# Kernel optimization log

Measured on AMD Instinct MI355X. Metric: run time of the kernel, lower is better.

Reference implementation:

```python
import jax, jax.numpy as jnp
import numpy as np

T_START = 0.0
T_END = 1.0
STEPS = 10
HID = 1024
BATCH = 8192


def setup_inputs() -> dict:
    key = jax.random.key(0)
    ks = jax.random.split(key, 7)
    s1 = 1.0 / np.sqrt(HID + 1)
    s2 = 1.0 / np.sqrt(HID)
    return {
        "h": jax.random.normal(ks[0], (BATCH, HID), dtype=jnp.float32),
        "W1": jax.random.uniform(ks[1], (HID + 1, HID), jnp.float32, -s1, s1),
        "b1": jax.random.uniform(ks[2], (HID,), jnp.float32, -s1, s1),
        "W2": jax.random.uniform(ks[3], (HID, HID), jnp.float32, -s2, s2),
        "b2": jax.random.uniform(ks[4], (HID,), jnp.float32, -s2, s2),
        "W3": jax.random.uniform(ks[5], (HID, HID), jnp.float32, -s2, s2),
        "b3": jax.random.uniform(ks[6], (HID,), jnp.float32, -s2, s2),
    }


def reference(h, W1, b1, W2, b2, W3, b3):
    dt = (T_END - T_START) / STEPS

    def dynamics(t, h):
        # concat(h, t*ones) @ W1 == h @ W1[:-1] + t * W1[-1]; keep explicit concat for clarity
        t_vec = jnp.full((h.shape[0], 1), t, dtype=h.dtype)
        x = jnp.concatenate([h, t_vec], axis=1)
        x = jnp.tanh(x @ W1 + b1)
        x = jnp.tanh(x @ W2 + b2)
        return x @ W3 + b3

    def rk4_step(h, t):
        k1 = dynamics(t, h)
        k2 = dynamics(t + dt / 2, h + dt / 2 * k1)
        k3 = dynamics(t + dt / 2, h + dt / 2 * k2)
        k4 = dynamics(t + dt, h + dt * k3)
        return h + dt / 6 * (k1 + 2 * k2 + 2 * k3 + k4), None

    ts = T_START + dt * jnp.arange(STEPS, dtype=h.dtype)
    h_final, _ = jax.lax.scan(rk4_step, h, ts)
    return h_final
```

## Files before the change

### kernel.cpp

```cpp
#include <hip/hip_runtime.h>


typedef __attribute__((ext_vector_type(8))) __bf16 bf16x8;
typedef __attribute__((ext_vector_type(4))) float f32x4;
typedef __attribute__((ext_vector_type(8))) float f32x8;
typedef __attribute__((ext_vector_type(16))) float f32x16;
typedef __attribute__((ext_vector_type(8))) unsigned short us8;
typedef __attribute__((ext_vector_type(4))) int i32x4;
typedef __attribute__((ext_vector_type(8))) int i32x8;
typedef unsigned short ushort_t;
typedef unsigned char u8;

#define SCALE_ONE  0x7F7F7F7Fu
#define SCALE_INV32 0x7A7A7A7Au

#define GLOAD16(gp, lp) \
  __builtin_amdgcn_global_load_lds((const __attribute__((address_space(1))) unsigned int*)(gp), \
                                   (__attribute__((address_space(3))) unsigned int*)(lp), 16, 0, 0)

__device__ __forceinline__ ushort_t f2bf(float f) {
  union { float f; unsigned u; } v; v.f = f;
  unsigned r = v.u + 0x7fffu + ((v.u >> 16) & 1u);
  return (ushort_t)(r >> 16);
}
__device__ __forceinline__ float b2f(ushort_t u) {
  union { unsigned u; float f; } v; v.u = ((unsigned)u) << 16; return v.f;
}
__device__ __forceinline__ float fast_tanh(float x) {
  float e = __expf(2.0f * x);
  return 1.0f - 2.0f * __builtin_amdgcn_rcpf(e + 1.0f);
}
__device__ __forceinline__ uint2 pack_fp8x8(const float* v) {
  int a = __builtin_amdgcn_cvt_pk_fp8_f32(v[0], v[1], 0, false);
  a = __builtin_amdgcn_cvt_pk_fp8_f32(v[2], v[3], a, true);
  int b = __builtin_amdgcn_cvt_pk_fp8_f32(v[4], v[5], 0, false);
  b = __builtin_amdgcn_cvt_pk_fp8_f32(v[6], v[7], b, true);
  return make_uint2((unsigned)a, (unsigned)b);
}
__device__ __forceinline__ void fp8x4_to_f32(unsigned q, float* o) {
  o[0] = __builtin_amdgcn_cvt_f32_fp8(q, 0);
  o[1] = __builtin_amdgcn_cvt_f32_fp8(q, 1);
  o[2] = __builtin_amdgcn_cvt_f32_fp8(q, 2);
  o[3] = __builtin_amdgcn_cvt_f32_fp8(q, 3);
}
__device__ __forceinline__ void fp8x8_to_f32(uint2 q, float* o) {
  fp8x4_to_f32(q.x, o); fp8x4_to_f32(q.y, o + 4);
}

__global__ void transpose_bf16(const float* __restrict__ in, ushort_t* __restrict__ out) {
  __shared__ float tile[32][33];
  const int bx = blockIdx.x * 32, by = blockIdx.y * 32;
  const int tx = threadIdx.x, ty = threadIdx.y;
#pragma unroll
  for (int i = 0; i < 32; i += 8)
    tile[ty + i][tx] = in[(size_t)(by + ty + i) * 1024 + bx + tx];
  __syncthreads();
#pragma unroll
  for (int i = 0; i < 32; i += 8)
    out[(size_t)(bx + ty + i) * 1024 + by + tx] = f2bf(tile[tx][ty + i]);
}

__global__ void transpose_fp8(const float* __restrict__ in, u8* __restrict__ out) {
  __shared__ float tile[32][33];
  const int bx = blockIdx.x * 32, by = blockIdx.y * 32;
  const int tx = threadIdx.x, ty = threadIdx.y;
#pragma unroll
  for (int i = 0; i < 32; i += 8)
    tile[ty + i][tx] = in[(size_t)(by + ty + i) * 1024 + bx + tx];
  __syncthreads();
#pragma unroll
  for (int i = 0; i < 32; i += 8) {
    const float v = 32.f * tile[tx][ty + i];
    int r = __builtin_amdgcn_cvt_pk_fp8_f32(v, v, 0, false);
    out[(size_t)(bx + ty + i) * 1024 + by + tx] = (u8)(r & 0xFF);
  }
}

__global__ void conv_bf16(const float* __restrict__ in, ushort_t* __restrict__ out) {
  size_t i = ((size_t)blockIdx.x * 256 + threadIdx.x) * 4;
  float4 v = *(const float4*)&in[i];
  ushort4 o;
  o.x = f2bf(v.x); o.y = f2bf(v.y); o.z = f2bf(v.z); o.w = f2bf(v.w);
  *(ushort4*)&out[i] = o;
}

__global__ void c31_kernel(const ushort_t* __restrict__ W1t, const float* __restrict__ b3,
                           float* __restrict__ c31) {
  const int j = blockIdx.x * 256 + threadIdx.x;
  float acc = 0.f;
  for (int c = 0; c < 128; ++c) {
    const us8 w = *(const us8*)&W1t[(size_t)j * 1024 + c * 8];
    const f32x8 b = *(const f32x8*)&b3[c * 8];
#pragma unroll
    for (int e = 0; e < 8; ++e) acc += b2f(w[e]) * b[e];
  }
  c31[j] = acc;
}

__global__ void xtfold(const u8* __restrict__ a, const u8* __restrict__ b,
                       const u8* __restrict__ c, const u8* __restrict__ d,
                       ushort_t* __restrict__ XT) {
  const size_t i = ((size_t)blockIdx.x * 256 + threadIdx.x) * 8;
  float va[8], vb[8], vc[8], vd[8];
  fp8x8_to_f32(*(const uint2*)&a[i], va);
  fp8x8_to_f32(*(const uint2*)&b[i], vb);
  fp8x8_to_f32(*(const uint2*)&c[i], vc);
  fp8x8_to_f32(*(const uint2*)&d[i], vd);
  const us8 xo = *(const us8*)&XT[i];
  us8 xn;
#pragma unroll
  for (int e = 0; e < 8; ++e)
    xn[e] = f2bf(b2f(xo[e]) + va[e] + 2.f * (vb[e] + vc[e]) + vd[e]);
  *(us8*)&XT[i] = xn;
}

template<int MODE>
__global__ void __launch_bounds__(256, 2)
gemm_bf16(const ushort_t* __restrict__ Ag, const ushort_t* __restrict__ Bg,
          const float* __restrict__ bias,
          ushort_t* __restrict__ outb, u8* __restrict__ out8,
          const float* __restrict__ h0f, float* __restrict__ outf)
{
  constexpr int K = 1024, NCOL = 1024, NT = 16;
  constexpr float DT = 0.1f;
  __shared__ __align__(16) ushort_t lds[2][16384];

  const int bid = blockIdx.x;
  const int nb = (int)gridDim.x >> 3;
  const int logical = (bid & 7) * nb + (bid >> 3);
  const int bm0 = (logical >> 3) * 128;
  const int bn0 = (logical & 7) * 128;

  const int tid = threadIdx.x;
  const int w = tid >> 6, l = tid & 63;
  const int wr = w >> 1, wc = w & 1;

  const int srow = l >> 3;
  const int sclog = (l & 7) ^ srow;
  const size_t gA0 = (size_t)(bm0 + w * 32 + srow) * K + sclog * 8;
  const size_t gB0 = (size_t)(bn0 + w * 32 + srow) * K + sclog * 8;
  const int ldsAo = w * 2048 + l * 8;
  const int ldsBo = 8192 + w * 2048 + l * 8;

#define STAGEB(s, t1) do { \
    const ushort_t* ga = Ag + gA0 + (size_t)(t1) * 64; \
    const ushort_t* gb = Bg + gB0 + (size_t)(t1) * 64; \
    GLOAD16(ga,          &lds[s][ldsAo]); \
    GLOAD16(ga + 8 * K,  &lds[s][ldsAo + 512]); \
    GLOAD16(ga + 16 * K, &lds[s][ldsAo + 1024]); \
    GLOAD16(ga + 24 * K, &lds[s][ldsAo + 1536]); \
    GLOAD16(gb,          &lds[s][ldsBo]); \
    GLOAD16(gb + 8 * K,  &lds[s][ldsBo + 512]); \
    GLOAD16(gb + 16 * K, &lds[s][ldsBo + 1024]); \
    GLOAD16(gb + 24 * K, &lds[s][ldsBo + 1536]); } while (0)

  const int r = l & 15, kb = l >> 4, xr = r & 7;
  const int aRow = (wr * 64 + r) * 64;
  const int bRow = 8192 + (wc * 64 + r) * 64;
  const int c0 = ((0 | kb) ^ xr) * 8;
  const int c1 = ((4 | kb) ^ xr) * 8;

  f32x4 acc[4][4];
#pragma unroll
  for (int m = 0; m < 4; ++m)
#pragma unroll
    for (int n = 0; n < 4; ++n) acc[m][n] = (f32x4){0.f, 0.f, 0.f, 0.f};

  STAGEB(0, 0);

  for (int t = 0; t < NT; ++t) {
    const int cur = t & 1;
    __builtin_amdgcn_s_barrier();
    if (t + 1 < NT) {
      STAGEB(cur ^ 1, t + 1);
      asm volatile("s_waitcnt vmcnt(8)" ::: "memory");
    } else {
      asm volatile("s_waitcnt vmcnt(0)" ::: "memory");
    }
    __builtin_amdgcn_s_barrier();
    __builtin_amdgcn_sched_barrier(0);

    const ushort_t* Lb = &lds[cur][0];
    bf16x8 av[4], bv[4];
#pragma unroll
    for (int m = 0; m < 4; ++m) av[m] = *(const bf16x8*)(Lb + aRow + m * 1024 + c0);
#pragma unroll
    for (int n = 0; n < 4; ++n) bv[n] = *(const bf16x8*)(Lb + bRow + n * 1024 + c0);
    __builtin_amdgcn_s_setprio(1);
#pragma unroll
    for (int m = 0; m < 4; ++m)
#pragma unroll
      for (int n = 0; n < 4; ++n)
        acc[m][n] = __builtin_amdgcn_mfma_f32_16x16x32_bf16(av[m], bv[n], acc[m][n], 0, 0, 0);
    __builtin_amdgcn_s_setprio(0);
#pragma unroll
    for (int m = 0; m < 4; ++m) av[m] = *(const bf16x8*)(Lb + aRow + m * 1024 + c1);
#pragma unroll
    for (int n = 0; n < 4; ++n) bv[n] = *(const bf16x8*)(Lb + bRow + n * 1024 + c1);
    __builtin_amdgcn_s_setprio(1);
#pragma unroll
    for (int m = 0; m < 4; ++m)
#pragma unroll
      for (int n = 0; n < 4; ++n)
        acc[m][n] = __builtin_amdgcn_mfma_f32_16x16x32_bf16(av[m], bv[n], acc[m][n], 0, 0, 0);
    __builtin_amdgcn_s_setprio(0);
  }
#undef STAGEB

  __syncthreads();
  ushort_t* C = &lds[0][0];
  const int er = (l >> 4) * 4;
  const int ec = l & 15;
#pragma unroll
  for (int n = 0; n < 4; ++n) {
    const int lc = wc * 64 + n * 16 + ec;
#pragma unroll
    for (int m = 0; m < 4; ++m) {
#pragma unroll
      for (int j = 0; j < 4; ++j) {
        const int lr = wr * 64 + m * 16 + er + j;
        C[lr * 136 + lc] = f2bf(acc[m][n][j]);
      }
    }
  }
  __syncthreads();

  constexpr float DT6 = DT / 6.f;
#pragma unroll
  for (int i = 0; i < 8; ++i) {
    const int chunk = tid + i * 256;
    const int row = chunk >> 4;
    const int cc = chunk & 15;
    const int col0 = bn0 + cc * 8;
    const us8 kv8 = *(const us8*)&C[row * 136 + cc * 8];
    const size_t gidx = (size_t)(bm0 + row) * NCOL + col0;

    if (MODE == 0) {
      float v[8];
#pragma unroll
      for (int e = 0; e < 8; ++e) v[e] = 32.f * b2f(kv8[e]);
      *(uint2*)&out8[gidx] = pack_fp8x8(v);
    } else if (MODE == 1) {
      const f32x8 b = *(const f32x8*)&bias[col0];
      float v[8];
#pragma unroll
      for (int e = 0; e < 8; ++e) v[e] = fast_tanh(b2f(kv8[e]) + b[e]);
      *(us8*)&outb[gidx] = kv8;
      *(uint2*)&out8[gidx] = pack_fp8x8(v);
    } else {
      const f32x8 b = *(const f32x8*)&bias[col0];
      const f32x8 h8 = *(const f32x8*)&h0f[gidx];
      f32x8 o;
#pragma unroll
      for (int e = 0; e < 8; ++e) o[e] = h8[e] + DT6 * b2f(kv8[e]) + b[e];
      *(f32x8*)&outf[gidx] = o;
    }
  }
}

template<int MODE>
__global__ void __launch_bounds__(256, 2)
gemm_fp8(const u8* __restrict__ Ag, const u8* __restrict__ Bg,
         const float* __restrict__ bias, const float* __restrict__ wl,
         const float* __restrict__ c31,
         const ushort_t* __restrict__ hW1r,
         const u8* __restrict__ g0p, const u8* __restrict__ g1p, const u8* __restrict__ g2p,
         const u8* __restrict__ x2a, const u8* __restrict__ x2b, const u8* __restrict__ x2c,
         u8* __restrict__ out8, u8* __restrict__ gout,
         ushort_t* __restrict__ bfio, ushort_t* __restrict__ hW1w,
         float p1, float p2, int flag)
{
  constexpr int NT = 8;
  constexpr float DT = 0.1f, DT6 = DT / 6.f;
  __shared__ __align__(16) u8 bufs[2][32768];

  const int bid = blockIdx.x;
  const int nb = (int)gridDim.x >> 3;
  const int logical = (bid & 7) * nb + (bid >> 3);
  const int bm0 = (logical >> 3) * 128;
  const int bn0 = (logical & 7) * 128;

  const int tid = threadIdx.x;
  const int w = tid >> 6, l = tid & 63;
  const int wr = w >> 1, wc = w & 1;
  const int l31 = l & 31, kg = l >> 5;

  int so[4], ldo[4];
#pragma unroll
  for (int i = 0; i < 4; ++i) {
    const int slot = tid + i * 256;
    const int row = slot >> 3, phys = slot & 7;
    so[i] = row * 1024 + ((phys ^ (row & 7)) << 4);
    ldo[i] = slot << 4;
  }
  const u8* gA = Ag + (size_t)bm0 * 1024;
  const u8* gB = Bg + (size_t)bn0 * 1024;

#define STAGEF(s, t1) do { \
    GLOAD16(gA + so[0] + (t1) * 128, &bufs[s][ldo[0]]); \
    GLOAD16(gA + so[1] + (t1) * 128, &bufs[s][ldo[1]]); \
    GLOAD16(gA + so[2] + (t1) * 128, &bufs[s][ldo[2]]); \
    GLOAD16(gA + so[3] + (t1) * 128, &bufs[s][ldo[3]]); \
    GLOAD16(gB + so[0] + (t1) * 128, &bufs[s][16384 + ldo[0]]); \
    GLOAD16(gB + so[1] + (t1) * 128, &bufs[s][16384 + ldo[1]]); \
    GLOAD16(gB + so[2] + (t1) * 128, &bufs[s][16384 + ldo[2]]); \
    GLOAD16(gB + so[3] + (t1) * 128, &bufs[s][16384 + ldo[3]]); } while (0)

  auto ldsAddr = [](int row, int c) -> int {
    return row * 128 + ((c ^ (row & 7)) << 4);
  };
  const int ra0 = wr * 64 + l31, ra1 = ra0 + 32;
  const int rb0 = wc * 64 + l31, rb1 = rb0 + 32;
  const int ck0 = kg * 2, ck1 = 4 + kg * 2;
  const int a00 = ldsAddr(ra0, ck0), a00b = ldsAddr(ra0, ck0 + 1);
  const int a10 = ldsAddr(ra1, ck0), a10b = ldsAddr(ra1, ck0 + 1);
  const int b00 = 16384 + ldsAddr(rb0, ck0), b00b = 16384 + ldsAddr(rb0, ck0 + 1);
  const int b10 = 16384 + ldsAddr(rb1, ck0), b10b = 16384 + ldsAddr(rb1, ck0 + 1);
  const int a01 = ldsAddr(ra0, ck1), a01b = ldsAddr(ra0, ck1 + 1);
  const int a11 = ldsAddr(ra1, ck1), a11b = ldsAddr(ra1, ck1 + 1);
  const int b01 = 16384 + ldsAddr(rb0, ck1), b01b = 16384 + ldsAddr(rb0, ck1 + 1);
  const int b11 = 16384 + ldsAddr(rb1, ck1), b11b = 16384 + ldsAddr(rb1, ck1 + 1);

  f32x16 acc00, acc01, acc10, acc11;
#pragma unroll
  for (int i = 0; i < 16; ++i) { acc00[i] = 0.f; acc01[i] = 0.f; acc10[i] = 0.f; acc11[i] = 0.f; }

#define LD8(dst, o0, o1) do { \
    i32x4 lo_ = *(const i32x4*)(Lb + (o0)); \
    i32x4 hi_ = *(const i32x4*)(Lb + (o1)); \
    dst = (i32x8){lo_[0], lo_[1], lo_[2], lo_[3], hi_[0], hi_[1], hi_[2], hi_[3]}; } while (0)

  STAGEF(0, 0);

  for (int t = 0; t < NT; ++t) {
    const int cur = t & 1;
    __builtin_amdgcn_s_barrier();
    if (t + 1 < NT) {
      STAGEF(cur ^ 1, t + 1);
      asm volatile("s_waitcnt vmcnt(8)" ::: "memory");
    } else {
      asm volatile("s_waitcnt vmcnt(0)" ::: "memory");
    }
    __builtin_amdgcn_s_barrier();
    __builtin_amdgcn_sched_barrier(0);

    const u8* Lb = &bufs[cur][0];
    i32x8 a0, a1, b0, b1;
    LD8(a0, a00, a00b);
    LD8(a1, a10, a10b);
    LD8(b0, b00, b00b);
    LD8(b1, b10, b10b);
    __builtin_amdgcn_s_setprio(1);
    acc00 = __builtin_amdgcn_mfma_scale_f32_32x32x64_f8f6f4(a0, b0, acc00, 0, 0, 0, SCALE_ONE, 0, SCALE_INV32);
    acc01 = __builtin_amdgcn_mfma_scale_f32_32x32x64_f8f6f4(a0, b1, acc01, 0, 0, 0, SCALE_ONE, 0, SCALE_INV32);
    acc10 = __builtin_amdgcn_mfma_scale_f32_32x32x64_f8f6f4(a1, b0, acc10, 0, 0, 0, SCALE_ONE, 0, SCALE_INV32);
    acc11 = __builtin_amdgcn_mfma_scale_f32_32x32x64_f8f6f4(a1, b1, acc11, 0, 0, 0, SCALE_ONE, 0, SCALE_INV32);
    __builtin_amdgcn_s_setprio(0);
    LD8(a0, a01, a01b);
    LD8(a1, a11, a11b);
    LD8(b0, b01, b01b);
    LD8(b1, b11, b11b);
    __builtin_amdgcn_s_setprio(1);
    acc00 = __builtin_amdgcn_mfma_scale_f32_32x32x64_f8f6f4(a0, b0, acc00, 0, 0, 0, SCALE_ONE, 0, SCALE_INV32);
    acc01 = __builtin_amdgcn_mfma_scale_f32_32x32x64_f8f6f4(a0, b1, acc01, 0, 0, 0, SCALE_ONE, 0, SCALE_INV32);
    acc10 = __builtin_amdgcn_mfma_scale_f32_32x32x64_f8f6f4(a1, b0, acc10, 0, 0, 0, SCALE_ONE, 0, SCALE_INV32);
    acc11 = __builtin_amdgcn_mfma_scale_f32_32x32x64_f8f6f4(a1, b1, acc11, 0, 0, 0, SCALE_ONE, 0, SCALE_INV32);
    __builtin_amdgcn_s_setprio(0);
  }
#undef STAGEF

  us8 hw_pre[8];
  if (MODE == 3 || MODE == 4) {
#pragma unroll
    for (int i = 0; i < 8; ++i) {
      const int chunk = tid + i * 256;
      const size_t gidx = (size_t)(bm0 + (chunk >> 4)) * 1024 + bn0 + (chunk & 15) * 8;
      hw_pre[i] = *(const us8*)&hW1r[gidx];
    }
  }
  uint2 g0_pre[8], g1_pre[8], g2_pre[8];
  if (MODE == 4) {
#pragma unroll
    for (int i = 0; i < 8; ++i) {
      const int chunk = tid + i * 256;
      const size_t gidx = (size_t)(bm0 + (chunk >> 4)) * 1024 + bn0 + (chunk & 15) * 8;
      g0_pre[i] = *(const uint2*)&g0p[gidx];
      g1_pre[i] = *(const uint2*)&g1p[gidx];
      g2_pre[i] = *(const uint2*)&g2p[gidx];
    }
  }

  __syncthreads();
  ushort_t* Cst = (ushort_t*)&bufs[0][0];
#define STORE_ACC(A_, mm, nn) do { \
    _Pragma("unroll") \
    for (int reg = 0; reg < 16; ++reg) { \
      const int lrow = wr * 64 + (mm) * 32 + (reg & 3) + 8 * (reg >> 2) + 4 * kg; \
      const int lcol = wc * 64 + (nn) * 32 + l31; \
      Cst[lrow * 136 + lcol] = f2bf(A_[reg]); } } while (0)
  STORE_ACC(acc00, 0, 0);
  STORE_ACC(acc01, 0, 1);
  STORE_ACC(acc10, 1, 0);
  STORE_ACC(acc11, 1, 1);
#undef STORE_ACC
  __syncthreads();

#pragma unroll
  for (int i = 0; i < 8; ++i) {
    const int chunk = tid + i * 256;
    const int row = chunk >> 4;
    const int cc = chunk & 15;
    const int col0 = bn0 + cc * 8;
    const us8 kv8 = *(const us8*)&Cst[row * 136 + cc * 8];
    const size_t gidx = (size_t)(bm0 + row) * 1024 + col0;

    if (MODE == 2) {
      const f32x8 b = *(const f32x8*)&bias[col0];
      float x2v[8];
#pragma unroll
      for (int e = 0; e < 8; ++e) x2v[e] = fast_tanh(b2f(kv8[e]) + b[e]);
      *(uint2*)&out8[gidx] = pack_fp8x8(x2v);
    } else if (MODE == 3) {
      const f32x8 b  = *(const f32x8*)&bias[col0];
      const f32x8 wv = *(const f32x8*)&wl[col0];
      const f32x8 cv = *(const f32x8*)&c31[col0];
      const us8 hw = hw_pre[i];
      float gv[8], x1v[8];
#pragma unroll
      for (int e = 0; e < 8; ++e) {
        gv[e] = b2f(kv8[e]);
        x1v[e] = fast_tanh(b2f(hw[e]) + p1 * (gv[e] + cv[e]) + b[e] + p2 * wv[e]);
      }
      *(uint2*)&gout[gidx] = pack_fp8x8(gv);
      *(uint2*)&out8[gidx] = pack_fp8x8(x1v);
    } else {
      const f32x8 b  = *(const f32x8*)&bias[col0];
      const f32x8 wv = *(const f32x8*)&wl[col0];
      const f32x8 cv = *(const f32x8*)&c31[col0];
      const us8 hw = hw_pre[i];
      float g0v[8], g1v[8], g2v[8];
      fp8x8_to_f32(g0_pre[i], g0v);
      fp8x8_to_f32(g1_pre[i], g1v);
      fp8x8_to_f32(g2_pre[i], g2v);
      float va[8], vb[8], vc[8], vd[8];
      fp8x8_to_f32(*(const uint2*)&x2a[gidx], va);
      fp8x8_to_f32(*(const uint2*)&x2b[gidx], vb);
      fp8x8_to_f32(*(const uint2*)&x2c[gidx], vc);
      fp8x8_to_f32(*(const uint2*)&Ag[gidx], vd);
      us8 xtn;
      if (flag) {
#pragma unroll
        for (int e = 0; e < 8; ++e)
          xtn[e] = f2bf(va[e] + 2.f * (vb[e] + vc[e]) + vd[e]);
      } else {
        const us8 xo = *(const us8*)&bfio[gidx];
#pragma unroll
        for (int e = 0; e < 8; ++e)
          xtn[e] = f2bf(b2f(xo[e]) + va[e] + 2.f * (vb[e] + vc[e]) + vd[e]);
      }
      *(us8*)&bfio[gidx] = xtn;
      float x1v[8]; us8 o1;
#pragma unroll
      for (int e = 0; e < 8; ++e) {
        const float gs = g0v[e] + 2.f * (g1v[e] + g2v[e]) + b2f(kv8[e]);
        const float hn = b2f(hw[e]) + DT6 * gs + DT * cv[e];
        o1[e] = f2bf(hn);
        x1v[e] = fast_tanh(hn + b[e] + p2 * wv[e]);
      }
      *(us8*)&hW1w[gidx] = o1;
      *(uint2*)&out8[gidx] = pack_fp8x8(x1v);
    }
  }
}

extern "C" void kernel_launch(void* const* d_in, const int* in_sizes, int n_in,
                              void* d_out, int out_size, void* d_ws, size_t ws_size,
                              hipStream_t stream) {
  (void)in_sizes; (void)n_in; (void)out_size; (void)ws_size;
  const float* h_in = (const float*)d_in[0];
  const float* W1   = (const float*)d_in[1];
  const float* b1   = (const float*)d_in[2];
  const float* W2   = (const float*)d_in[3];
  const float* b2   = (const float*)d_in[4];
  const float* W3   = (const float*)d_in[5];
  const float* b3   = (const float*)d_in[6];
  const float* W1last = W1 + (size_t)1024 * 1024;

  char* ws = (char*)d_ws;
  ushort_t* W1t   = (ushort_t*)(ws);
  u8*       W2t8  = (u8*)      (ws + (2ull << 20));
  u8*       Bt318 = (u8*)      (ws + (3ull << 20));
  float*    c31   = (float*)   (ws + (4ull << 20));
  ushort_t* hW1b  = (ushort_t*)(ws + (8ull << 20));
  u8*       x1    = (u8*)      (ws + (24ull << 20));
  u8*       x2s0  = (u8*)      (ws + (32ull << 20));
  u8*       x2s1  = (u8*)      (ws + (40ull << 20));
  u8*       x2s2  = (u8*)      (ws + (48ull << 20));
  u8*       x2s3  = (u8*)      (ws + (56ull << 20));
  ushort_t* XT    = (ushort_t*)(ws + (64ull << 20));
  u8*       g0    = (u8*)d_out;
  u8*       g1    = (u8*)d_out + (8ull << 20);
  u8*       g2    = (u8*)d_out + (16ull << 20);
  ushort_t* hb    = (ushort_t*)d_out;
  float*    OUT   = (float*)d_out;

  const float dt = 0.1f;
  constexpr int GRID = 512, BLK = 256;
  dim3 tb(32, 8), tg(32, 32);

  transpose_bf16<<<tg, tb, 0, stream>>>(W1, W1t);
  transpose_fp8 <<<tg, tb, 0, stream>>>(W2, W2t8);
  conv_bf16<<<1024, 256, 0, stream>>>(W3, XT);
  conv_bf16<<<8192, 256, 0, stream>>>(h_in, hb);
  c31_kernel<<<4, 256, 0, stream>>>(W1t, b3, c31);
  gemm_bf16<0><<<64, BLK, 0, stream>>>(W1t, XT, nullptr, nullptr, Bt318, nullptr, nullptr);
  gemm_bf16<1><<<GRID, BLK, 0, stream>>>(hb, W1t, b1, hW1b, x1, nullptr, nullptr);

  for (int step = 0; step < 10; ++step) {
    const float t0 = step * dt;
    gemm_fp8<2><<<GRID, BLK, 0, stream>>>(x1, W2t8, b2, nullptr, nullptr, nullptr,
                                          nullptr, nullptr, nullptr, nullptr, nullptr, nullptr,
                                          x2s0, nullptr, nullptr, nullptr, 0.f, 0.f, 0);
    gemm_fp8<3><<<GRID, BLK, 0, stream>>>(x2s0, Bt318, b1, W1last, c31, hW1b,
                                          nullptr, nullptr, nullptr, nullptr, nullptr, nullptr,
                                          x1, g0, nullptr, nullptr, 0.5f * dt, t0 + 0.5f * dt, 0);
    gemm_fp8<2><<<GRID, BLK, 0, stream>>>(x1, W2t8, b2, nullptr, nullptr, nullptr,
                                          nullptr, nullptr, nullptr, nullptr, nullptr, nullptr,
                                          x2s1, nullptr, nullptr, nullptr, 0.f, 0.f, 0);
    gemm_fp8<3><<<GRID, BLK, 0, stream>>>(x2s1, Bt318, b1, W1last, c31, hW1b,
                                          nullptr, nullptr, nullptr, nullptr, nullptr, nullptr,
                                          x1, g1, nullptr, nullptr, 0.5f * dt, t0 + 0.5f * dt, 0);
    gemm_fp8<2><<<GRID, BLK, 0, stream>>>(x1, W2t8, b2, nullptr, nullptr, nullptr,
                                          nullptr, nullptr, nullptr, nullptr, nullptr, nullptr,
                                          x2s2, nullptr, nullptr, nullptr, 0.f, 0.f, 0);
    gemm_fp8<3><<<GRID, BLK, 0, stream>>>(x2s2, Bt318, b1, W1last, c31, hW1b,
                                          nullptr, nullptr, nullptr, nullptr, nullptr, nullptr,
                                          x1, g2, nullptr, nullptr, dt, t0 + dt, 0);
    gemm_fp8<2><<<GRID, BLK, 0, stream>>>(x1, W2t8, b2, nullptr, nullptr, nullptr,
                                          nullptr, nullptr, nullptr, nullptr, nullptr, nullptr,
                                          x2s3, nullptr, nullptr, nullptr, 0.f, 0.f, 0);
    if (step < 9) {
      gemm_fp8<4><<<GRID, BLK, 0, stream>>>(x2s3, Bt318, b1, W1last, c31, hW1b,
                                            g0, g1, g2, x2s0, x2s1, x2s2,
                                            x1, nullptr, XT, hW1b,
                                            0.f, t0 + dt, (step == 0));
    }
  }
  xtfold<<<4096, 256, 0, stream>>>(x2s0, x2s1, x2s2, x2s3, XT);

  transpose_bf16<<<tg, tb, 0, stream>>>(W3, W1t);
  gemm_bf16<5><<<GRID, BLK, 0, stream>>>(XT, W1t, b3, nullptr, nullptr, h_in, OUT);
}
```

Measured before the change: 1.447 ms.

## Pre-swizzle FP8 weight fragments and load B directly to registers

Adds a one-time swizzle kernel that rearranges the FP8 weight matrices into per-lane MFMA fragment order. The GEMM then loads B fragments straight from global memory into registers, prefetching one k-step ahead, and stages only A through LDS. This halves LDS traffic and removes the B LDS reads. In exchange each wave reads B from global/L2 independently rather than sharing it through LDS, and register pressure goes up.

```diff
diff --git a/kernel.cpp b/kernel.cpp
--- a/kernel.cpp
+++ b/kernel.cpp
@@ -74,6 +74,18 @@
     int r = __builtin_amdgcn_cvt_pk_fp8_f32(v, v, 0, false);
     out[(size_t)(bx + ty + i) * 1024 + by + tx] = (u8)(r & 0xFF);
   }
+}
+
+__global__ void swizzleB(const u8* __restrict__ src, u8* __restrict__ dst) {
+  const int c = blockIdx.x * 256 + threadIdx.x;
+  const int lane = c & 63, r = c >> 6;
+  const int half = r & 1, wcq = (r >> 1) & 1, kb = (r >> 2) & 1;
+  const int t = (r >> 3) & 7, bn = r >> 6;
+  const int row = bn * 128 + wcq * 64 + half * 32 + (lane & 31);
+  const int col = t * 128 + kb * 64 + (lane >> 5) * 32;
+  const uint4* s = (const uint4*)(src + (size_t)row * 1024 + col);
+  uint4* d = (uint4*)(dst + (size_t)c * 32);
+  d[0] = s[0]; d[1] = s[1];
 }
 
 __global__ void conv_bf16(const float* __restrict__ in, ushort_t* __restrict__ out) {
@@ -260,7 +272,7 @@
 
 template<int MODE>
 __global__ void __launch_bounds__(256, 2)
-gemm_fp8(const u8* __restrict__ Ag, const u8* __restrict__ Bg,
+gemm_fp8(const u8* __restrict__ Ag, const u8* __restrict__ Bf,
          const float* __restrict__ bias, const float* __restrict__ wl,
          const float* __restrict__ c31,
          const ushort_t* __restrict__ hW1r,
@@ -272,11 +284,11 @@
 {
   constexpr int NT = 8;
   constexpr float DT = 0.1f, DT6 = DT / 6.f;
-  __shared__ __align__(16) u8 bufs[2][32768];
+  __shared__ __align__(16) u8 ldsraw[36864];
 
   const int bid = blockIdx.x;
-  const int nb = (int)gridDim.x >> 3;
-  const int logical = (bid & 7) * nb + (bid >> 3);
+  const int nbq = (int)gridDim.x >> 3;
+  const int logical = (bid & 7) * nbq + (bid >> 3);
   const int bm0 = (logical >> 3) * 128;
   const int bn0 = (logical & 7) * 128;
 
@@ -294,32 +306,26 @@
     ldo[i] = slot << 4;
   }
   const u8* gA = Ag + (size_t)bm0 * 1024;
-  const u8* gB = Bg + (size_t)bn0 * 1024;
-
-#define STAGEF(s, t1) do { \
-    GLOAD16(gA + so[0] + (t1) * 128, &bufs[s][ldo[0]]); \
-    GLOAD16(gA + so[1] + (t1) * 128, &bufs[s][ldo[1]]); \
-    GLOAD16(gA + so[2] + (t1) * 128, &bufs[s][ldo[2]]); \
-    GLOAD16(gA + so[3] + (t1) * 128, &bufs[s][ldo[3]]); \
-    GLOAD16(gB + so[0] + (t1) * 128, &bufs[s][16384 + ldo[0]]); \
-    GLOAD16(gB + so[1] + (t1) * 128, &bufs[s][16384 + ldo[1]]); \
-    GLOAD16(gB + so[2] + (t1) * 128, &bufs[s][16384 + ldo[2]]); \
-    GLOAD16(gB + so[3] + (t1) * 128, &bufs[s][16384 + ldo[3]]); } while (0)
+
+#define STAGEA(s, t1) do { \
+    u8* base = ldsraw + (s) * 16384; \
+    GLOAD16(gA + so[0] + (t1) * 128, base + ldo[0]); \
+    GLOAD16(gA + so[1] + (t1) * 128, base + ldo[1]); \
+    GLOAD16(gA + so[2] + (t1) * 128, base + ldo[2]); \
+    GLOAD16(gA + so[3] + (t1) * 128, base + ldo[3]); } while (0)
 
   auto ldsAddr = [](int row, int c) -> int {
     return row * 128 + ((c ^ (row & 7)) << 4);
   };
   const int ra0 = wr * 64 + l31, ra1 = ra0 + 32;
-  const int rb0 = wc * 64 + l31, rb1 = rb0 + 32;
   const int ck0 = kg * 2, ck1 = 4 + kg * 2;
   const int a00 = ldsAddr(ra0, ck0), a00b = ldsAddr(ra0, ck0 + 1);
   const int a10 = ldsAddr(ra1, ck0), a10b = ldsAddr(ra1, ck0 + 1);
-  const int b00 = 16384 + ldsAddr(rb0, ck0), b00b = 16384 + ldsAddr(rb0, ck0 + 1);
-  const int b10 = 16384 + ldsAddr(rb1, ck0), b10b = 16384 + ldsAddr(rb1, ck0 + 1);
   const int a01 = ldsAddr(ra0, ck1), a01b = ldsAddr(ra0, ck1 + 1);
   const int a11 = ldsAddr(ra1, ck1), a11b = ldsAddr(ra1, ck1 + 1);
-  const int b01 = 16384 + ldsAddr(rb0, ck1), b01b = 16384 + ldsAddr(rb0, ck1 + 1);
-  const int b11 = 16384 + ldsAddr(rb1, ck1), b11b = 16384 + ldsAddr(rb1, ck1 + 1);
+
+  const u8* Bfb = Bf + (size_t)(bn0 >> 7) * 131072 + wc * 4096 + l * 32;
+#define BFRAG(t1, kbq, h) (*(const i32x8*)(Bfb + (t1) * 16384 + (kbq) * 8192 + (h) * 2048))
 
   f32x16 acc00, acc01, acc10, acc11;
 #pragma unroll
@@ -330,44 +336,48 @@
     i32x4 hi_ = *(const i32x4*)(Lb + (o1)); \
     dst = (i32x8){lo_[0], lo_[1], lo_[2], lo_[3], hi_[0], hi_[1], hi_[2], hi_[3]}; } while (0)
 
-  STAGEF(0, 0);
-
+  STAGEA(0, 0);
+  i32x8 bf0 = BFRAG(0, 0, 0), bf1 = BFRAG(0, 0, 1);
+  i32x8 bf2 = BFRAG(0, 1, 0), bf3 = BFRAG(0, 1, 1);
+
+#pragma unroll
   for (int t = 0; t < NT; ++t) {
     const int cur = t & 1;
+    i32x8 nb0, nb1, nb2, nb3;
     __builtin_amdgcn_s_barrier();
     if (t + 1 < NT) {
-      STAGEF(cur ^ 1, t + 1);
-      asm volatile("s_waitcnt vmcnt(8)" ::: "memory");
+      STAGEA(cur ^ 1, t + 1);
+      nb0 = BFRAG(t + 1, 0, 0); nb1 = BFRAG(t + 1, 0, 1);
+      nb2 = BFRAG(t + 1, 1, 0); nb3 = BFRAG(t + 1, 1, 1);
+      asm volatile("s_waitcnt vmcnt(12)" ::: "memory");
     } else {
       asm volatile("s_waitcnt vmcnt(0)" ::: "memory");
     }
     __builtin_amdgcn_s_barrier();
     __builtin_amdgcn_sched_barrier(0);
 
-    const u8* Lb = &bufs[cur][0];
-    i32x8 a0, a1, b0, b1;
+    const u8* Lb = ldsraw + cur * 16384;
+    i32x8 a0, a1;
     LD8(a0, a00, a00b);
     LD8(a1, a10, a10b);
-    LD8(b0, b00, b00b);
-    LD8(b1, b10, b10b);
     __builtin_amdgcn_s_setprio(1);
-    acc00 = __builtin_amdgcn_mfma_scale_f32_32x32x64_f8f6f4(a0, b0, acc00, 0, 0, 0, SCALE_ONE, 0, SCALE_INV32);
-    acc01 = __builtin_amdgcn_mfma_scale_f32_32x32x64_f8f6f4(a0, b1, acc01, 0, 0, 0, SCALE_ONE, 0, SCALE_INV32);
-    acc10 = __builtin_amdgcn_mfma_scale_f32_32x32x64_f8f6f4(a1, b0, acc10, 0, 0, 0, SCALE_ONE, 0, SCALE_INV32);
-    acc11 = __builtin_amdgcn_mfma_scale_f32_32x32x64_f8f6f4(a1, b1, acc11, 0, 0, 0, SCALE_ONE, 0, SCALE_INV32);
+    acc00 = __builtin_amdgcn_mfma_scale_f32_32x32x64_f8f6f4(a0, bf0, acc00, 0, 0, 0, SCALE_ONE, 0, SCALE_INV32);
+    acc01 = __builtin_amdgcn_mfma_scale_f32_32x32x64_f8f6f4(a0, bf1, acc01, 0, 0, 0, SCALE_ONE, 0, SCALE_INV32);
+    acc10 = __builtin_amdgcn_mfma_scale_f32_32x32x64_f8f6f4(a1, bf0, acc10, 0, 0, 0, SCALE_ONE, 0, SCALE_INV32);
+    acc11 = __builtin_amdgcn_mfma_scale_f32_32x32x64_f8f6f4(a1, bf1, acc11, 0, 0, 0, SCALE_ONE, 0, SCALE_INV32);
     __builtin_amdgcn_s_setprio(0);
     LD8(a0, a01, a01b);
     LD8(a1, a11, a11b);
-    LD8(b0, b01, b01b);
-    LD8(b1, b11, b11b);
     __builtin_amdgcn_s_setprio(1);
-    acc00 = __builtin_amdgcn_mfma_scale_f32_32x32x64_f8f6f4(a0, b0, acc00, 0, 0, 0, SCALE_ONE, 0, SCALE_INV32);
-    acc01 = __builtin_amdgcn_mfma_scale_f32_32x32x64_f8f6f4(a0, b1, acc01, 0, 0, 0, SCALE_ONE, 0, SCALE_INV32);
-    acc10 = __builtin_amdgcn_mfma_scale_f32_32x32x64_f8f6f4(a1, b0, acc10, 0, 0, 0, SCALE_ONE, 0, SCALE_INV32);
-    acc11 = __builtin_amdgcn_mfma_scale_f32_32x32x64_f8f6f4(a1, b1, acc11, 0, 0, 0, SCALE_ONE, 0, SCALE_INV32);
+    acc00 = __builtin_amdgcn_mfma_scale_f32_32x32x64_f8f6f4(a0, bf2, acc00, 0, 0, 0, SCALE_ONE, 0, SCALE_INV32);
+    acc01 = __builtin_amdgcn_mfma_scale_f32_32x32x64_f8f6f4(a0, bf3, acc01, 0, 0, 0, SCALE_ONE, 0, SCALE_INV32);
+    acc10 = __builtin_amdgcn_mfma_scale_f32_32x32x64_f8f6f4(a1, bf2, acc10, 0, 0, 0, SCALE_ONE, 0, SCALE_INV32);
+    acc11 = __builtin_amdgcn_mfma_scale_f32_32x32x64_f8f6f4(a1, bf3, acc11, 0, 0, 0, SCALE_ONE, 0, SCALE_INV32);
     __builtin_amdgcn_s_setprio(0);
-  }
-#undef STAGEF
+    bf0 = nb0; bf1 = nb1; bf2 = nb2; bf3 = nb3;
+  }
+#undef STAGEA
+#undef BFRAG
 
   us8 hw_pre[8];
   if (MODE == 3 || MODE == 4) {
@@ -391,7 +401,7 @@
   }
 
   __syncthreads();
-  ushort_t* Cst = (ushort_t*)&bufs[0][0];
+  ushort_t* Cst = (ushort_t*)&ldsraw[0];
 #define STORE_ACC(A_, mm, nn) do { \
     _Pragma("unroll") \
     for (int reg = 0; reg < 16; ++reg) { \
@@ -491,6 +501,8 @@
   u8*       W2t8  = (u8*)      (ws + (2ull << 20));
   u8*       Bt318 = (u8*)      (ws + (3ull << 20));
   float*    c31   = (float*)   (ws + (4ull << 20));
+  u8*       W2f   = (u8*)      (ws + (5ull << 20));
+  u8*       B31f  = (u8*)      (ws + (6ull << 20));
   ushort_t* hW1b  = (ushort_t*)(ws + (8ull << 20));
   u8*       x1    = (u8*)      (ws + (24ull << 20));
   u8*       x2s0  = (u8*)      (ws + (32ull << 20));
@@ -514,33 +526,35 @@
   conv_bf16<<<8192, 256, 0, stream>>>(h_in, hb);
   c31_kernel<<<4, 256, 0, stream>>>(W1t, b3, c31);
   gemm_bf16<0><<<64, BLK, 0, stream>>>(W1t, XT, nullptr, nullptr, Bt318, nullptr, nullptr);
+  swizzleB<<<128, 256, 0, stream>>>(W2t8, W2f);
+  swizzleB<<<128, 256, 0, stream>>>(Bt318, B31f);
   gemm_bf16<1><<<GRID, BLK, 0, stream>>>(hb, W1t, b1, hW1b, x1, nullptr, nullptr);
 
   for (int step = 0; step < 10; ++step) {
     const float t0 = step * dt;
-    gemm_fp8<2><<<GRID, BLK, 0, stream>>>(x1, W2t8, b2, nullptr, nullptr, nullptr,
+    gemm_fp8<2><<<GRID, BLK, 0, stream>>>(x1, W2f, b2, nullptr, nullptr, nullptr,
                                           nullptr, nullptr, nullptr, nullptr, nullptr, nullptr,
                                           x2s0, nullptr, nullptr, nullptr, 0.f, 0.f, 0);
-    gemm_fp8<3><<<GRID, BLK, 0, stream>>>(x2s0, Bt318, b1, W1last, c31, hW1b,
+    gemm_fp8<3><<<GRID, BLK, 0, stream>>>(x2s0, B31f, b1, W1last, c31, hW1b,
                                           nullptr, nullptr, nullptr, nullptr, nullptr, nullptr,
                                           x1, g0, nullptr, nullptr, 0.5f * dt, t0 + 0.5f * dt, 0);
-    gemm_fp8<2><<<GRID, BLK, 0, stream>>>(x1, W2t8, b2, nullptr, nullptr, nullptr,
+    gemm_fp8<2><<<GRID, BLK, 0, stream>>>(x1, W2f, b2, nullptr, nullptr, nullptr,
                                           nullptr, nullptr, nullptr, nullptr, nullptr, nullptr,
                                           x2s1, nullptr, nullptr, nullptr, 0.f, 0.f, 0);
-    gemm_fp8<3><<<GRID, BLK, 0, stream>>>(x2s1, Bt318, b1, W1last, c31, hW1b,
+    gemm_fp8<3><<<GRID, BLK, 0, stream>>>(x2s1, B31f, b1, W1last, c31, hW1b,
                                           nullptr, nullptr, nullptr, nullptr, nullptr, nullptr,
                                           x1, g1, nullptr, nullptr, 0.5f * dt, t0 + 0.5f * dt, 0);
-    gemm_fp8<2><<<GRID, BLK, 0, stream>>>(x1, W2t8, b2, nullptr, nullptr, nullptr,
+    gemm_fp8<2><<<GRID, BLK, 0, stream>>>(x1, W2f, b2, nullptr, nullptr, nullptr,
                                           nullptr, nullptr, nullptr, nullptr, nullptr, nullptr,
                                           x2s2, nullptr, nullptr, nullptr, 0.f, 0.f, 0);
-    gemm_fp8<3><<<GRID, BLK, 0, stream>>>(x2s2, Bt318, b1, W1last, c31, hW1b,
+    gemm_fp8<3><<<GRID, BLK, 0, stream>>>(x2s2, B31f, b1, W1last, c31, hW1b,
                                           nullptr, nullptr, nullptr, nullptr, nullptr, nullptr,
                                           x1, g2, nullptr, nullptr, dt, t0 + dt, 0);
-    gemm_fp8<2><<<GRID, BLK, 0, stream>>>(x1, W2t8, b2, nullptr, nullptr, nullptr,
+    gemm_fp8<2><<<GRID, BLK, 0, stream>>>(x1, W2f, b2, nullptr, nullptr, nullptr,
                                           nullptr, nullptr, nullptr, nullptr, nullptr, nullptr,
                                           x2s3, nullptr, nullptr, nullptr, 0.f, 0.f, 0);
     if (step < 9) {
-      gemm_fp8<4><<<GRID, BLK, 0, stream>>>(x2s3, Bt318, b1, W1last, c31, hW1b,
+      gemm_fp8<4><<<GRID, BLK, 0, stream>>>(x2s3, B31f, b1, W1last, c31, hW1b,
                                             g0, g1, g2, x2s0, x2s1, x2s2,
                                             x1, nullptr, XT, hW1b,
                                             0.f, t0 + dt, (step == 0));
```

Measured after the change: 1.458 ms. No clear change (+0.8%).
